# Kernel tuning notes

Measured on AMD Instinct MI355X. Metric: run time of the kernel, lower is better.

## Reference

```python
import jax, jax.numpy as jnp
import numpy as np

N, E, F, H, O, G = 50000, 800000, 50, 512, 121, 20
EPS = 1e-5


def _lin(k, out_f, in_f):
    return jax.random.normal(k, (out_f, in_f), jnp.float32) / np.sqrt(in_f)


def setup_inputs() -> dict:
    key = jax.random.key(0)
    ks = jax.random.split(key, 32)
    inp = {
        "x": jax.random.normal(ks[0], (N, F), jnp.float32),
        "edge_index": jax.random.randint(ks[1], (2, E), 0, N, jnp.int64 if jax.config.jax_enable_x64 else jnp.int32),
        "batch": jnp.sort(jax.random.randint(ks[2], (N,), 0, G, jnp.int32)),
    }
    dims = [(F, H), (H, H), (H, H), (H, H), (H, O)]
    ki = 3
    for i, (fi, fo) in enumerate(dims, start=1):
        inp[f"W{i}l"] = _lin(ks[ki], fo, fi); ki += 1
        inp[f"W{i}r"] = _lin(ks[ki], fo, fi); ki += 1
        inp[f"b{i}"] = jnp.zeros((fo,), jnp.float32)
    for i in range(1, 5):
        inp[f"g{i}"] = jnp.ones((H,), jnp.float32)    # GraphNorm weight
        inp[f"bn{i}"] = jnp.zeros((H,), jnp.float32)  # GraphNorm bias
        inp[f"a{i}"] = jnp.ones((H,), jnp.float32)    # GraphNorm mean_scale
    return inp


def _sage(x, src, dst, inv_deg, Wl, Wr, b):
    # mean aggregation of neighbor messages x[src] at dst, then two linears
    agg = jax.ops.segment_sum(x[src], dst, num_segments=N) * inv_deg  # [N, Fin]
    return agg @ Wl.T + x @ Wr.T + b


def _gnorm(x, batch, inv_sz, w, b, alpha):
    mean = jax.ops.segment_sum(x, batch, num_segments=G) * inv_sz  # [G, C]
    out = x - alpha * mean[batch]
    var = jax.ops.segment_sum(out * out, batch, num_segments=G) * inv_sz
    return out * jax.lax.rsqrt(var[batch] + EPS) * w + b


def reference(x, edge_index, batch,
              W1l, W1r, b1, W2l, W2r, b2, W3l, W3r, b3, W4l, W4r, b4, W5l, W5r, b5,
              g1, bn1, a1, g2, bn2, a2, g3, bn3, a3, g4, bn4, a4):
    src, dst = edge_index[0], edge_index[1]
    deg = jax.ops.segment_sum(jnp.ones((E,), jnp.float32), dst, num_segments=N)
    inv_deg = (1.0 / jnp.maximum(deg, 1.0))[:, None]
    sz = jax.ops.segment_sum(jnp.ones((N,), jnp.float32), batch, num_segments=G)
    inv_sz = (1.0 / jnp.maximum(sz, 1.0))[:, None]

    h = _sage(x, src, dst, inv_deg, W1l, W1r, b1)
    h = jax.nn.relu(_gnorm(h, batch, inv_sz, g1, bn1, a1))  # dropout=identity (eval)
    h = _sage(h, src, dst, inv_deg, W2l, W2r, b2)
    h = jax.nn.relu(_gnorm(h, batch, inv_sz, g2, bn2, a2))
    h = _sage(h, src, dst, inv_deg, W3l, W3r, b3)
    h = jax.nn.relu(_gnorm(h, batch, inv_sz, g3, bn3, a3))
    h = _sage(h, src, dst, inv_deg, W4l, W4r, b4)
    h = jax.nn.relu(_gnorm(h, batch, inv_sz, g4, bn4, a4))
    return _sage(h, src, dst, inv_deg, W5l, W5r, b5)
```

## Files before the change

kernel.cpp:

```cpp
#include <hip/hip_runtime.h>
#include <cstddef>
#include <cstdint>

#define N_NODES 50000
#define N_EDGES 800000
#define F_IN 50
#define K1PAD 64
#define H_DIM 512
#define O_DIM 121
#define N_GROUPS 20
#define EPSV 1e-5f
#define M_PAD 50048
#define M_TILES 391

#define SCAN_BLK 256
#define SCAN_NBLK ((N_NODES + SCAN_BLK - 1) / SCAN_BLK)
#define WALL_EL 1769472
#define XB_EL (M_PAD * K1PAD)

typedef unsigned short u16;
typedef __attribute__((ext_vector_type(8))) short short8;
typedef __attribute__((ext_vector_type(8))) unsigned short u16x8;
typedef __attribute__((ext_vector_type(4))) float f32x4;

__device__ __forceinline__ float b2f(u16 u) {
  union { unsigned int i; float f; } v; v.i = ((unsigned int)u) << 16; return v.f;
}
__device__ __forceinline__ u16 f2b(float f) {
  union { float f; unsigned int i; } v; v.f = f;
  unsigned int x = v.i;
  return (u16)((x + 0x7fffu + ((x >> 16) & 1u)) >> 16);
}

__device__ __forceinline__ void gl_lds16(const void* g, void* l) {
  __builtin_amdgcn_global_load_lds(
      (__attribute__((address_space(1))) void*)(g),
      (__attribute__((address_space(3))) void*)(l), 16, 0, 0);
}


__global__ void k_deg(const int* __restrict__ dst, int* __restrict__ deg) {
  int e = blockIdx.x * blockDim.x + threadIdx.x;
  if (e < N_EDGES) atomicAdd(&deg[dst[e]], 1);
}

__global__ void k_scan1(const int* __restrict__ deg, int* __restrict__ off,
                        int* __restrict__ bsum) {
  __shared__ int buf[SCAN_BLK];
  int gid = blockIdx.x * SCAN_BLK + threadIdx.x;
  buf[threadIdx.x] = (gid < N_NODES) ? deg[gid] : 0;
  __syncthreads();
  for (int d = 1; d < SCAN_BLK; d <<= 1) {
    int t = (threadIdx.x >= d) ? buf[threadIdx.x - d] : 0;
    __syncthreads();
    buf[threadIdx.x] += t;
    __syncthreads();
  }
  if (gid < N_NODES) off[gid + 1] = buf[threadIdx.x];
  if (threadIdx.x == SCAN_BLK - 1) bsum[blockIdx.x] = buf[threadIdx.x];
}

__global__ void k_scan2_gbounds(int* __restrict__ bsum, const int* __restrict__ batch,
                                int* __restrict__ gstart, float* __restrict__ inv_sz) {
  int t = threadIdx.x;
  if (blockIdx.x == 0) {
    __shared__ int buf[256];
    buf[t] = (t < SCAN_NBLK) ? bsum[t] : 0;
    __syncthreads();
    for (int d = 1; d < 256; d <<= 1) {
      int v = (t >= d) ? buf[t - d] : 0;
      __syncthreads();
      buf[t] += v;
      __syncthreads();
    }
    if (t < SCAN_NBLK) bsum[t] = buf[t];
  } else {
    if (t <= N_GROUPS) {
      int lo = 0, hi = N_NODES;
      while (lo < hi) {
        int mid = (lo + hi) >> 1;
        if (batch[mid] < t) lo = mid + 1; else hi = mid;
      }
      gstart[t] = lo;
    }
    __syncthreads();
    if (t < N_GROUPS) {
      int sz = gstart[t + 1] - gstart[t];
      inv_sz[t] = 1.0f / (float)max(sz, 1);
    }
  }
}

__global__ void k_scan3prep(int* __restrict__ off, const int* __restrict__ bsum,
                            const int* __restrict__ deg, float* __restrict__ inv_deg,
                            int* __restrict__ cursor) {
  int gid = blockIdx.x * SCAN_BLK + threadIdx.x;
  if (gid < N_NODES) {
    int add = (blockIdx.x > 0) ? bsum[blockIdx.x - 1] : 0;
    int v = off[gid + 1] + add;
    off[gid + 1] = v;
    if (gid + 1 < N_NODES) cursor[gid + 1] = v;
    inv_deg[gid] = 1.0f / (float)max(deg[gid], 1);
  }
  if (gid == 0) { off[0] = 0; cursor[0] = 0; }
}

__global__ void k_scatter(const int* __restrict__ src, const int* __restrict__ dst,
                          int* __restrict__ cursor, int* __restrict__ csr_src) {
  int e = blockIdx.x * blockDim.x + threadIdx.x;
  if (e < N_EDGES) {
    int p = atomicAdd(&cursor[dst[e]], 1);
    csr_src[p] = src[e];
  }
}

struct WcSrc { const float* p[10]; };
__global__ void k_convert_all(const float* __restrict__ x, WcSrc s,
                              u16* __restrict__ xb, u16* __restrict__ wall) {
  int idx = blockIdx.x * blockDim.x + threadIdx.x;
  if (idx < XB_EL) {
    int r = idx >> 6, c = idx & (K1PAD - 1);
    float v = (r < N_NODES && c < F_IN) ? x[r * F_IN + c] : 0.f;
    xb[idx] = f2b(v);
    return;
  }
  idx -= XB_EL;
  if (idx >= WALL_EL) return;
  const int seg_start[10] = {0, 32768, 65536, 327680, 589824, 851968,
                             1114112, 1376256, 1638400, 1703936};
  const int jr[10]  = {512, 512, 512, 512, 512, 512, 512, 512, 121, 121};
  const int kin[10] = {50, 50, 512, 512, 512, 512, 512, 512, 512, 512};
  const int ksh[10] = {6, 6, 9, 9, 9, 9, 9, 9, 9, 9};
  int sgi = 0;
#pragma unroll
  for (int t = 1; t < 10; ++t)
    if (idx >= seg_start[t]) sgi = t;
  int local = idx - seg_start[sgi];
  int j = local >> ksh[sgi];
  int k = local & ((1 << ksh[sgi]) - 1);
  float v = (j < jr[sgi] && k < kin[sgi]) ? s.p[sgi][j * kin[sgi] + k] : 0.f;
  wall[idx] = f2b(v);
}


__global__ void k_agg_small(const u16* __restrict__ xb, const int* __restrict__ off,
                            const int* __restrict__ srcs, const float* __restrict__ inv_deg,
                            u16* __restrict__ agg) {
  int n = blockIdx.x;
  int f = threadIdx.x;
  int b = off[n], e = off[n + 1];
  float s = 0.f;
  for (int i = b; i < e; ++i) s += b2f(xb[(size_t)srcs[i] * K1PAD + f]);
  agg[(size_t)n * K1PAD + f] = f2b(s * inv_deg[n]);
}

__global__ __launch_bounds__(512) void k_agg512(
    const u16* __restrict__ h, const int* __restrict__ off,
    const int* __restrict__ srcs, const float* __restrict__ inv_deg,
    u16* __restrict__ agg) {
  __shared__ float part[4][64][8];
  int slot = threadIdx.y >> 1;
  int sub = threadIdx.y & 1;
  int n = blockIdx.x * 4 + slot;
  int t = threadIdx.x;
  float a[8] = {0.f, 0.f, 0.f, 0.f, 0.f, 0.f, 0.f, 0.f};
  if (n < N_NODES) {
    int b = off[n], e = off[n + 1];
    int half = (e - b + 1) >> 1;
    int lo = b + sub * half;
    int hi = min(lo + half, e);
    int i = lo;
    for (; i + 4 <= hi; i += 4) {
      u16x8 v0 = ((const u16x8*)(h + (size_t)srcs[i + 0] * H_DIM))[t];
      u16x8 v1 = ((const u16x8*)(h + (size_t)srcs[i + 1] * H_DIM))[t];
      u16x8 v2 = ((const u16x8*)(h + (size_t)srcs[i + 2] * H_DIM))[t];
      u16x8 v3 = ((const u16x8*)(h + (size_t)srcs[i + 3] * H_DIM))[t];
#pragma unroll
      for (int j = 0; j < 8; ++j)
        a[j] += (b2f(v0[j]) + b2f(v1[j])) + (b2f(v2[j]) + b2f(v3[j]));
    }
    for (; i < hi; ++i) {
      u16x8 v0 = ((const u16x8*)(h + (size_t)srcs[i] * H_DIM))[t];
#pragma unroll
      for (int j = 0; j < 8; ++j) a[j] += b2f(v0[j]);
    }
  }
  if (sub == 1) {
#pragma unroll
    for (int j = 0; j < 8; ++j) part[slot][t][j] = a[j];
  }
  __syncthreads();
  if (sub == 0 && n < N_NODES) {
    float w = inv_deg[n];
    u16x8 r;
#pragma unroll
    for (int j = 0; j < 8; ++j) r[j] = f2b((a[j] + part[slot][t][j]) * w);
    ((u16x8*)(agg + (size_t)n * H_DIM))[t] = r;
  }
}

__global__ __launch_bounds__(256) void k_agg_final(
    const u16* __restrict__ Plb, const float* __restrict__ Prf,
    const int* __restrict__ off, const int* __restrict__ srcs,
    const float* __restrict__ inv_deg, const float* __restrict__ bias,
    float* __restrict__ out) {
  int n = blockIdx.x * 8 + (threadIdx.x >> 5);
  if (n >= N_NODES) return;
  int l = threadIdx.x & 31;
  int c0 = l * 4;
  int b = off[n], e = off[n + 1];
  float a0 = 0.f, a1 = 0.f, a2 = 0.f, a3 = 0.f;
  int i = b;
  for (; i + 2 <= e; i += 2) {
    ushort4 v0 = ((const ushort4*)(Plb + (size_t)srcs[i] * 128))[l];
    ushort4 v1 = ((const ushort4*)(Plb + (size_t)srcs[i + 1] * 128))[l];
    a0 += b2f(v0.x) + b2f(v1.x); a1 += b2f(v0.y) + b2f(v1.y);
    a2 += b2f(v0.z) + b2f(v1.z); a3 += b2f(v0.w) + b2f(v1.w);
  }
  if (i < e) {
    ushort4 v0 = ((const ushort4*)(Plb + (size_t)srcs[i] * 128))[l];
    a0 += b2f(v0.x); a1 += b2f(v0.y); a2 += b2f(v0.z); a3 += b2f(v0.w);
  }
  float w = inv_deg[n];
  float4 pr = ((const float4*)(Prf + (size_t)n * 128))[l];
  float r0 = a0 * w + pr.x, r1 = a1 * w + pr.y;
  float r2 = a2 * w + pr.z, r3 = a3 * w + pr.w;
  size_t ob = (size_t)n * O_DIM;
  if (c0 + 0 < O_DIM) out[ob + c0 + 0] = r0 + bias[c0 + 0];
  if (c0 + 1 < O_DIM) out[ob + c0 + 1] = r1 + bias[c0 + 1];
  if (c0 + 2 < O_DIM) out[ob + c0 + 2] = r2 + bias[c0 + 2];
  if (c0 + 3 < O_DIM) out[ob + c0 + 3] = r3 + bias[c0 + 3];
}


#define TM 128
#define TK 32

template <int JB, bool DUAL, int OUTMODE>
__global__ __launch_bounds__(256, 4) void k_gemm_mfma(
    const u16* __restrict__ A, const u16* __restrict__ X,
    const u16* __restrict__ Wl, const u16* __restrict__ Wr,
    const float* __restrict__ bias, void* __restrict__ C0,
    void* __restrict__ C1, const int* __restrict__ batch,
    float* __restrict__ ssum, float* __restrict__ ssq, int K) {
  __shared__ u16 As[TM * TK];
  __shared__ u16 Ls[TM * TK];
  __shared__ u16 Xs[DUAL ? TM * TK : 1];
  __shared__ u16 Rs[DUAL ? TM * TK : 1];

  int id = blockIdx.x;
  const int nfull = (M_TILES >> 3) * 8 * JB;
  int m_t, j_t;
  if (id < nfull) {
    m_t = (id / (8 * JB)) * 8 + (id & 7);
    j_t = (id >> 3) & (JB - 1);
  } else {
    int rem = id - nfull;
    const int nrem = M_TILES & 7;
    m_t = (M_TILES & ~7) + rem % nrem;
    j_t = rem / nrem;
  }
  int m0 = m_t * TM;
  int j0 = j_t * 128;

  int tid = threadIdx.x;
  int lane = tid & 63;
  int wave = tid >> 6;
  int quad = lane >> 4;
  int lr = lane & 15;
  int wm = (wave & 1) * 64;
  int wn = (wave >> 1) * 64;

  f32x4 acc[4][4] = {};

  int sr = tid >> 2;
  int sc = (tid & 3) * 8;
  size_t moff0 = (size_t)(m0 + sr) * K + sc;
  size_t moff1 = moff0 + (size_t)64 * K;
  size_t joff0 = (size_t)(j0 + sr) * K + sc;
  size_t joff1 = joff0 + (size_t)64 * K;
  const int dofs = tid * 8;

  for (int k0 = 0; k0 < K; k0 += TK) {
    __syncthreads();
    gl_lds16(A + moff0 + k0, As + dofs);
    gl_lds16(A + moff1 + k0, As + 2048 + dofs);
    gl_lds16(Wl + joff0 + k0, Ls + dofs);
    gl_lds16(Wl + joff1 + k0, Ls + 2048 + dofs);
    if constexpr (DUAL) {
      gl_lds16(X + moff0 + k0, Xs + dofs);
      gl_lds16(X + moff1 + k0, Xs + 2048 + dofs);
      gl_lds16(Wr + joff0 + k0, Rs + dofs);
      gl_lds16(Wr + joff1 + k0, Rs + 2048 + dofs);
    }
    __syncthreads();
    {
      short8 af[4], lf[4];
#pragma unroll
      for (int t = 0; t < 4; ++t) {
        af[t] = *(const short8*)(As + (wm + t * 16 + lr) * TK + quad * 8);
        lf[t] = *(const short8*)(Ls + (wn + t * 16 + lr) * TK + quad * 8);
      }
#pragma unroll
      for (int ti = 0; ti < 4; ++ti)
#pragma unroll
        for (int tj = 0; tj < 4; ++tj)
          acc[ti][tj] = __builtin_amdgcn_mfma_f32_16x16x32_bf16(
              af[ti], lf[tj], acc[ti][tj], 0, 0, 0);
    }
    if constexpr (DUAL) {
      short8 xf[4], rf[4];
#pragma unroll
      for (int t = 0; t < 4; ++t) {
        xf[t] = *(const short8*)(Xs + (wm + t * 16 + lr) * TK + quad * 8);
        rf[t] = *(const short8*)(Rs + (wn + t * 16 + lr) * TK + quad * 8);
      }
#pragma unroll
      for (int ti = 0; ti < 4; ++ti)
#pragma unroll
        for (int tj = 0; tj < 4; ++tj)
          acc[ti][tj] = __builtin_amdgcn_mfma_f32_16x16x32_bf16(
              xf[ti], rf[tj], acc[ti][tj], 0, 0, 0);
    }
  }

  if constexpr (OUTMODE == 0) {
    int glo = batch[m0];
    int lastrow = m0 + TM - 1;
    bool fast = (lastrow < N_NODES) && (batch[lastrow] == glo);
#pragma unroll
    for (int tj = 0; tj < 4; ++tj) {
      int gcol = j0 + wn + tj * 16 + lr;
      float bv = bias[gcol];
      float s = 0.f, q = 0.f;
#pragma unroll
      for (int ti = 0; ti < 4; ++ti) {
        f32x4 v = acc[ti][tj];
        int rbase = m0 + wm + ti * 16 + quad * 4;
        if (fast) {
#pragma unroll
          for (int r = 0; r < 4; ++r) {
            float val = v[r] + bv;
            ((u16*)C0)[(size_t)(rbase + r) * H_DIM + gcol] = f2b(val);
            s += val; q += val * val;
          }
        } else {
          if (rbase + 3 < N_NODES && batch[rbase] == batch[rbase + 3]) {
            float s4 = 0.f, q4 = 0.f;
#pragma unroll
            for (int r = 0; r < 4; ++r) {
              float val = v[r] + bv;
              ((u16*)C0)[(size_t)(rbase + r) * H_DIM + gcol] = f2b(val);
              s4 += val; q4 += val * val;
            }
            int g = batch[rbase];
            atomicAdd(&ssum[g * H_DIM + gcol], s4);
            atomicAdd(&ssq[g * H_DIM + gcol], q4);
          } else {
#pragma unroll
            for (int r = 0; r < 4; ++r) {
              int grow = rbase + r;
              if (grow < N_NODES) {
                float val = v[r] + bv;
                ((u16*)C0)[(size_t)grow * H_DIM + gcol] = f2b(val);
                int g = batch[grow];
                atomicAdd(&ssum[g * H_DIM + gcol], val);
                atomicAdd(&ssq[g * H_DIM + gcol], val * val);
              }
            }
          }
        }
      }
      if (fast) {
        s += __shfl_xor(s, 16); s += __shfl_xor(s, 32);
        q += __shfl_xor(q, 16); q += __shfl_xor(q, 32);
        if (quad == 0) {
          atomicAdd(&ssum[glo * H_DIM + gcol], s);
          atomicAdd(&ssq[glo * H_DIM + gcol], q);
        }
      }
    }
  } else {
#pragma unroll
    for (int tj = 0; tj < 4; ++tj) {
      int gcol = j0 + wn + tj * 16 + lr;
#pragma unroll
      for (int ti = 0; ti < 4; ++ti) {
        f32x4 v = acc[ti][tj];
#pragma unroll
        for (int r = 0; r < 4; ++r) {
          int grow = m0 + wm + ti * 16 + quad * 4 + r;
          if (gcol < 128)
            ((u16*)C0)[(size_t)grow * 128 + gcol] = f2b(v[r]);
          else
            ((float*)C1)[(size_t)grow * 128 + (gcol - 128)] = v[r];
        }
      }
    }
  }
}


__global__ void k_precomp(const float* __restrict__ ssum, const float* __restrict__ ssq,
                          const float* __restrict__ inv_sz, const float* __restrict__ gw,
                          const float* __restrict__ gb, const float* __restrict__ alpha,
                          float* __restrict__ S, float* __restrict__ T) {
  int idx = blockIdx.x * blockDim.x + threadIdx.x;
  if (idx >= N_GROUPS * H_DIM) return;
  int g = idx >> 9;
  int c = idx & (H_DIM - 1);
  float is = inv_sz[g];
  float m = ssum[idx] * is;
  float a = alpha[c];
  float var = fmaxf(ssq[idx] * is - a * (2.f - a) * m * m, 0.f);
  float inv = rsqrtf(var + EPSV);
  float sc = inv * gw[c];
  S[idx] = sc;
  T[idx] = gb[c] - a * m * sc;
}

__global__ void k_apply(u16* __restrict__ h, const int* __restrict__ batch,
                        const float* __restrict__ S, const float* __restrict__ T) {
  int tid = blockIdx.x * blockDim.x + threadIdx.x;
  if (tid >= N_NODES * (H_DIM / 8)) return;
  int n = tid >> 6;
  int c0 = (tid & 63) << 3;
  int g = batch[n];
  u16x8 hv = *(const u16x8*)(h + (size_t)n * H_DIM + c0);
  u16x8 out;
#pragma unroll
  for (int j = 0; j < 8; ++j) {
    int f = c0 + j;
    float y = b2f(hv[j]) * S[g * H_DIM + f] + T[g * H_DIM + f];
    out[j] = f2b(fmaxf(y, 0.f));
  }
  *(u16x8*)(h + (size_t)n * H_DIM + c0) = out;
}


extern "C" void kernel_launch(void* const* d_in, const int* in_sizes, int n_in,
                              void* d_out, int out_size, void* d_ws, size_t ws_size,
                              hipStream_t stream) {
  const float* x = (const float*)d_in[0];
  const int* edge = (const int*)d_in[1];
  const int* batch = (const int*)d_in[2];
  const float *Wl[5], *Wr[5], *bb[5];
  for (int i = 0; i < 5; ++i) {
    Wl[i] = (const float*)d_in[3 + 3 * i];
    Wr[i] = (const float*)d_in[4 + 3 * i];
    bb[i] = (const float*)d_in[5 + 3 * i];
  }
  const float *gamma[4], *beta[4], *alpha[4];
  for (int i = 0; i < 4; ++i) {
    gamma[i] = (const float*)d_in[18 + 3 * i];
    beta[i]  = (const float*)d_in[19 + 3 * i];
    alpha[i] = (const float*)d_in[20 + 3 * i];
  }
  const int* srcv = edge;
  const int* dstv = edge + N_EDGES;

  char* base = (char*)d_ws;
  size_t off = 0;
  auto carve = [&](size_t bytes) -> char* {
    char* p = base + off;
    off = (off + bytes + 255) & ~(size_t)255;
    return p;
  };
  int* deg       = (int*)carve((size_t)N_NODES * 4);
  float* inv_deg = (float*)carve((size_t)N_NODES * 4);
  int* csr_off   = (int*)carve((size_t)(N_NODES + 1) * 4);
  int* cursor    = (int*)carve((size_t)N_NODES * 4);
  int* csr_src   = (int*)carve((size_t)N_EDGES * 4);
  int* bsum      = (int*)carve((size_t)SCAN_NBLK * 4);
  int* gstart    = (int*)carve((size_t)(N_GROUPS + 1) * 4);
  float* inv_sz  = (float*)carve((size_t)N_GROUPS * 4);
  float* stats   = (float*)carve((size_t)4 * 2 * N_GROUPS * H_DIM * 4);
  float* Sbuf    = (float*)carve((size_t)N_GROUPS * H_DIM * 4);
  float* Tbuf    = (float*)carve((size_t)N_GROUPS * H_DIM * 4);
  u16* xb        = (u16*)carve((size_t)XB_EL * 2);
  u16* aggx      = (u16*)carve((size_t)XB_EL * 2);
  u16* h0        = (u16*)carve((size_t)M_PAD * H_DIM * 2);
  u16* h1        = (u16*)carve((size_t)M_PAD * H_DIM * 2);
  u16* h2        = (u16*)carve((size_t)M_PAD * H_DIM * 2);
  u16* wall      = (u16*)carve((size_t)WALL_EL * 2);
  (void)ws_size; (void)in_sizes; (void)n_in; (void)out_size;

  u16* w1lb = wall;
  u16* w1rb = wall + 32768;
  u16* w2lb = wall + 65536;
  u16* w2rb = wall + 327680;
  u16* w3lb = wall + 589824;
  u16* w3rb = wall + 851968;
  u16* w4lb = wall + 1114112;
  u16* w4rb = wall + 1376256;
  u16* w5cat = wall + 1638400;

  u16* Plb = h1;
  float* Prf = (float*)((char*)h1 + (size_t)M_PAD * 128 * 2);

  hipMemsetAsync(deg, 0, (size_t)N_NODES * 4, stream);
  k_deg<<<(N_EDGES + 255) / 256, 256, 0, stream>>>(dstv, deg);
  k_scan1<<<SCAN_NBLK, SCAN_BLK, 0, stream>>>(deg, csr_off, bsum);
  k_scan2_gbounds<<<2, 256, 0, stream>>>(bsum, batch, gstart, inv_sz);
  k_scan3prep<<<SCAN_NBLK, SCAN_BLK, 0, stream>>>(csr_off, bsum, deg, inv_deg, cursor);
  k_scatter<<<(N_EDGES + 255) / 256, 256, 0, stream>>>(srcv, dstv, cursor, csr_src);

  WcSrc ws_src;
  ws_src.p[0] = Wl[0]; ws_src.p[1] = Wr[0];
  ws_src.p[2] = Wl[1]; ws_src.p[3] = Wr[1];
  ws_src.p[4] = Wl[2]; ws_src.p[5] = Wr[2];
  ws_src.p[6] = Wl[3]; ws_src.p[7] = Wr[3];
  ws_src.p[8] = Wl[4]; ws_src.p[9] = Wr[4];
  k_convert_all<<<(XB_EL + WALL_EL + 255) / 256, 256, 0, stream>>>(x, ws_src, xb, wall);

  hipMemsetAsync(stats, 0, (size_t)4 * 2 * N_GROUPS * H_DIM * 4, stream);

  const int nblk_main = M_TILES * 4;
  const int nblk_l5   = M_TILES * 2;
  dim3 aggblk(64, 8);
  int aggrid = (N_NODES + 3) / 4;

  auto norm = [&](u16* h, int l) {
    float* ss = stats + (size_t)l * 2 * N_GROUPS * H_DIM;
    float* sq = ss + N_GROUPS * H_DIM;
    k_precomp<<<(N_GROUPS * H_DIM + 255) / 256, 256, 0, stream>>>(
        ss, sq, inv_sz, gamma[l], beta[l], alpha[l], Sbuf, Tbuf);
    k_apply<<<(N_NODES * (H_DIM / 8) + 255) / 256, 256, 0, stream>>>(
        h, batch, Sbuf, Tbuf);
  };
  auto stat_ptr = [&](int l) { return stats + (size_t)l * 2 * N_GROUPS * H_DIM; };

  k_agg_small<<<N_NODES, 64, 0, stream>>>(xb, csr_off, csr_src, inv_deg, aggx);
  k_gemm_mfma<4, true, 0><<<nblk_main, 256, 0, stream>>>(
      aggx, xb, w1lb, w1rb, bb[0], h0, nullptr, batch,
      stat_ptr(0), stat_ptr(0) + N_GROUPS * H_DIM, K1PAD);
  norm(h0, 0);

  k_agg512<<<aggrid, aggblk, 0, stream>>>(h0, csr_off, csr_src, inv_deg, h1);
  k_gemm_mfma<4, true, 0><<<nblk_main, 256, 0, stream>>>(
      h1, h0, w2lb, w2rb, bb[1], h2, nullptr, batch,
      stat_ptr(1), stat_ptr(1) + N_GROUPS * H_DIM, H_DIM);
  norm(h2, 1);

  k_agg512<<<aggrid, aggblk, 0, stream>>>(h2, csr_off, csr_src, inv_deg, h0);
  k_gemm_mfma<4, true, 0><<<nblk_main, 256, 0, stream>>>(
      h0, h2, w3lb, w3rb, bb[2], h1, nullptr, batch,
      stat_ptr(2), stat_ptr(2) + N_GROUPS * H_DIM, H_DIM);
  norm(h1, 2);

  k_agg512<<<aggrid, aggblk, 0, stream>>>(h1, csr_off, csr_src, inv_deg, h2);
  k_gemm_mfma<4, true, 0><<<nblk_main, 256, 0, stream>>>(
      h2, h1, w4lb, w4rb, bb[3], h0, nullptr, batch,
      stat_ptr(3), stat_ptr(3) + N_GROUPS * H_DIM, H_DIM);
  norm(h0, 3);

  k_gemm_mfma<2, false, 1><<<nblk_l5, 256, 0, stream>>>(
      h0, nullptr, w5cat, nullptr, nullptr, Plb, Prf, nullptr, nullptr, nullptr, H_DIM);
  k_agg_final<<<(N_NODES + 7) / 8, 256, 0, stream>>>(
      Plb, Prf, csr_off, csr_src, inv_deg, bb[4], (float*)d_out);
}
```

Measured before the change: 1.071 ms.

## Add 256x256-tile 8-wave MFMA GEMM with interleaved double-buffered staging

Adds a new GEMM kernel using 256x256 output tiles and 512 threads, with double-buffered LDS and staged global-to-LDS loads interleaved between four MFMA sub-phases. It replaces the older GEMM for layers 2-4 and the final projection, and pads M to a multiple of 256. Larger tiles raise arithmetic intensity and cut operand reloads. The cost is higher register and LDS pressure and fewer blocks (392 for the main layers), which may under-fill the device and cause tail imbalance.

```diff
diff --git a/kernel.cpp b/kernel.cpp
--- a/kernel.cpp
+++ b/kernel.cpp
@@ -10,8 +10,9 @@
 #define O_DIM 121
 #define N_GROUPS 20
 #define EPSV 1e-5f
-#define M_PAD 50048
-#define M_TILES 391
+#define M_PAD 50176
+#define M_TILES 392
+#define M_TILES256 196
 
 #define SCAN_BLK 256
 #define SCAN_NBLK ((N_NODES + SCAN_BLK - 1) / SCAN_BLK)
@@ -396,6 +397,240 @@
             ((float*)C1)[(size_t)grow * 128 + (gcol - 128)] = v[r];
         }
       }
+    }
+  }
+}
+
+
+template <int OUTMODE>
+__global__ __launch_bounds__(512, 2) void k_gemm256(
+    const u16* __restrict__ Aa, const u16* __restrict__ Ax,
+    const u16* __restrict__ Bl, const u16* __restrict__ Br,
+    const float* __restrict__ bias, void* __restrict__ C0,
+    void* __restrict__ C1, const int* __restrict__ batch,
+    float* __restrict__ ssum, float* __restrict__ ssq, int knt) {
+  __shared__ u16 LA[2][256][64];
+  __shared__ u16 LB[2][256][64];
+
+  int m_t, j_t;
+  if constexpr (OUTMODE == 0) {
+    int lg = (blockIdx.x & 7) * 49 + (blockIdx.x >> 3);
+    m_t = lg >> 1; j_t = lg & 1;
+  } else {
+    m_t = blockIdx.x; j_t = 0;
+  }
+  const int m0 = m_t << 8;
+  const int j0 = j_t << 8;
+
+  const int tid = threadIdx.x;
+  const int lane = tid & 63;
+  const int wave = tid >> 6;
+  const int lr = lane & 15;
+  const int quad = lane >> 4;
+  const int wr64 = ((wave >> 2) & 1) << 6;
+  const int wc64 = (wave & 3) << 6;
+  const int rtid = tid >> 3;
+  const int sw = ((tid & 7) ^ (rtid & 7)) << 3;
+  const int c16_0 = (quad << 3) ^ ((lr & 7) << 3);
+  const int c16_1 = (32 + (quad << 3)) ^ ((lr & 7) << 3);
+
+  f32x4 acc[2][4][4] = {};
+  short8 af[4][2];
+  short8 bf[4][2];
+
+  auto STAGE = [&](int tt, int kind) {
+    if (tt >= knt) return;
+    const int bb = tt & 1;
+    const int ktl = (tt & 7) << 6;
+    if (kind <= 1) {
+      const u16* src = (tt >= 8) ? Ax : Aa;
+      const int r0 = kind << 7;
+      const u16* s0 = src + (size_t)(m0 + r0 + rtid) * 512 + ktl + sw;
+      u16* d = &LA[bb][r0][0] + tid * 8;
+      gl_lds16(s0, d);
+      gl_lds16(s0 + (size_t)64 * 512, d + 4096);
+    } else {
+      const u16* src = (tt >= 8) ? Br : Bl;
+      const int r0 = (kind - 2) << 7;
+      const u16* s0 = src + (size_t)(j0 + r0 + rtid) * 512 + ktl + sw;
+      u16* d = &LB[bb][r0][0] + tid * 8;
+      gl_lds16(s0, d);
+      gl_lds16(s0 + (size_t)64 * 512, d + 4096);
+    }
+  };
+
+  STAGE(0, 0); STAGE(0, 2); STAGE(0, 3); STAGE(0, 1);
+  STAGE(1, 0); STAGE(1, 2); STAGE(1, 3);
+  asm volatile("s_waitcnt vmcnt(6)" ::: "memory");
+  __builtin_amdgcn_s_barrier();
+
+  for (int t = 0; t < knt; ++t) {
+    const int b = t & 1;
+    const u16* ABase = &LA[b][0][0];
+    const u16* BBase = &LB[b][0][0];
+    const u16* abr = ABase + (size_t)(wr64 + lr) * 64;
+    const u16* bbr = BBase + (size_t)(wc64 + lr) * 64;
+
+#pragma unroll
+    for (int mi = 0; mi < 4; ++mi) {
+      af[mi][0] = *(const short8*)(abr + mi * 1024 + c16_0);
+      af[mi][1] = *(const short8*)(abr + mi * 1024 + c16_1);
+    }
+#pragma unroll
+    for (int nj = 0; nj < 2; ++nj) {
+      bf[nj][0] = *(const short8*)(bbr + nj * 1024 + c16_0);
+      bf[nj][1] = *(const short8*)(bbr + nj * 1024 + c16_1);
+    }
+    STAGE(t + 1, 1);
+    __builtin_amdgcn_s_barrier();
+    __builtin_amdgcn_s_setprio(1);
+#pragma unroll
+    for (int mi = 0; mi < 4; ++mi)
+#pragma unroll
+      for (int nj = 0; nj < 2; ++nj) {
+        acc[0][mi][nj] = __builtin_amdgcn_mfma_f32_16x16x32_bf16(
+            af[mi][0], bf[nj][0], acc[0][mi][nj], 0, 0, 0);
+        acc[0][mi][nj] = __builtin_amdgcn_mfma_f32_16x16x32_bf16(
+            af[mi][1], bf[nj][1], acc[0][mi][nj], 0, 0, 0);
+      }
+    __builtin_amdgcn_s_setprio(0);
+    __builtin_amdgcn_s_barrier();
+
+#pragma unroll
+    for (int nj = 2; nj < 4; ++nj) {
+      bf[nj][0] = *(const short8*)(bbr + nj * 1024 + c16_0);
+      bf[nj][1] = *(const short8*)(bbr + nj * 1024 + c16_1);
+    }
+    STAGE(t + 2, 0);
+    __builtin_amdgcn_s_barrier();
+    __builtin_amdgcn_s_setprio(1);
+#pragma unroll
+    for (int mi = 0; mi < 4; ++mi)
+#pragma unroll
+      for (int nj = 2; nj < 4; ++nj) {
+        acc[0][mi][nj] = __builtin_amdgcn_mfma_f32_16x16x32_bf16(
+            af[mi][0], bf[nj][0], acc[0][mi][nj], 0, 0, 0);
+        acc[0][mi][nj] = __builtin_amdgcn_mfma_f32_16x16x32_bf16(
+            af[mi][1], bf[nj][1], acc[0][mi][nj], 0, 0, 0);
+      }
+    __builtin_amdgcn_s_setprio(0);
+    __builtin_amdgcn_s_barrier();
+
+#pragma unroll
+    for (int mi = 0; mi < 4; ++mi) {
+      af[mi][0] = *(const short8*)(abr + 8192 + mi * 1024 + c16_0);
+      af[mi][1] = *(const short8*)(abr + 8192 + mi * 1024 + c16_1);
+    }
+    STAGE(t + 2, 2);
+    __builtin_amdgcn_s_barrier();
+    __builtin_amdgcn_s_setprio(1);
+#pragma unroll
+    for (int mi = 0; mi < 4; ++mi)
+#pragma unroll
+      for (int nj = 0; nj < 2; ++nj) {
+        acc[1][mi][nj] = __builtin_amdgcn_mfma_f32_16x16x32_bf16(
+            af[mi][0], bf[nj][0], acc[1][mi][nj], 0, 0, 0);
+        acc[1][mi][nj] = __builtin_amdgcn_mfma_f32_16x16x32_bf16(
+            af[mi][1], bf[nj][1], acc[1][mi][nj], 0, 0, 0);
+      }
+    __builtin_amdgcn_s_setprio(0);
+    __builtin_amdgcn_s_barrier();
+
+    STAGE(t + 2, 3);
+    if (t < knt - 2) {
+      asm volatile("s_waitcnt vmcnt(6)" ::: "memory");
+    } else if (t == knt - 2) {
+      asm volatile("s_waitcnt vmcnt(0)" ::: "memory");
+    }
+    __builtin_amdgcn_s_barrier();
+    __builtin_amdgcn_s_setprio(1);
+#pragma unroll
+    for (int mi = 0; mi < 4; ++mi)
+#pragma unroll
+      for (int nj = 2; nj < 4; ++nj) {
+        acc[1][mi][nj] = __builtin_amdgcn_mfma_f32_16x16x32_bf16(
+            af[mi][0], bf[nj][0], acc[1][mi][nj], 0, 0, 0);
+        acc[1][mi][nj] = __builtin_amdgcn_mfma_f32_16x16x32_bf16(
+            af[mi][1], bf[nj][1], acc[1][mi][nj], 0, 0, 0);
+      }
+    __builtin_amdgcn_s_setprio(0);
+    __builtin_amdgcn_s_barrier();
+  }
+
+  if constexpr (OUTMODE == 0) {
+    int glo = batch[m0];
+    int lastrow = m0 + 255;
+    bool fast = (lastrow < N_NODES) && (batch[lastrow] == glo);
+#pragma unroll
+    for (int nj = 0; nj < 4; ++nj) {
+      int gcol = j0 + wc64 + nj * 16 + lr;
+      float bv = bias[gcol];
+      float s = 0.f, q = 0.f;
+#pragma unroll
+      for (int band = 0; band < 2; ++band)
+#pragma unroll
+        for (int mi = 0; mi < 4; ++mi) {
+          f32x4 v = acc[band][mi][nj];
+          int rbase = m0 + band * 128 + wr64 + mi * 16 + quad * 4;
+          if (fast) {
+#pragma unroll
+            for (int r = 0; r < 4; ++r) {
+              float val = v[r] + bv;
+              ((u16*)C0)[(size_t)(rbase + r) * H_DIM + gcol] = f2b(val);
+              s += val; q += val * val;
+            }
+          } else if (rbase + 3 < N_NODES && batch[rbase] == batch[rbase + 3]) {
+            float s4 = 0.f, q4 = 0.f;
+#pragma unroll
+            for (int r = 0; r < 4; ++r) {
+              float val = v[r] + bv;
+              ((u16*)C0)[(size_t)(rbase + r) * H_DIM + gcol] = f2b(val);
+              s4 += val; q4 += val * val;
+            }
+            int g = batch[rbase];
+            atomicAdd(&ssum[g * H_DIM + gcol], s4);
+            atomicAdd(&ssq[g * H_DIM + gcol], q4);
+          } else {
+#pragma unroll
+            for (int r = 0; r < 4; ++r) {
+              int grow = rbase + r;
+              if (grow < N_NODES) {
+                float val = v[r] + bv;
+                ((u16*)C0)[(size_t)grow * H_DIM + gcol] = f2b(val);
+                int g = batch[grow];
+                atomicAdd(&ssum[g * H_DIM + gcol], val);
+                atomicAdd(&ssq[g * H_DIM + gcol], val * val);
+              }
+            }
+          }
+        }
+      if (fast) {
+        s += __shfl_xor(s, 16); s += __shfl_xor(s, 32);
+        q += __shfl_xor(q, 16); q += __shfl_xor(q, 32);
+        if (quad == 0) {
+          atomicAdd(&ssum[glo * H_DIM + gcol], s);
+          atomicAdd(&ssq[glo * H_DIM + gcol], q);
+        }
+      }
+    }
+  } else {
+#pragma unroll
+    for (int nj = 0; nj < 4; ++nj) {
+      int gcol = wc64 + nj * 16 + lr;
+#pragma unroll
+      for (int band = 0; band < 2; ++band)
+#pragma unroll
+        for (int mi = 0; mi < 4; ++mi) {
+          f32x4 v = acc[band][mi][nj];
+#pragma unroll
+          for (int r = 0; r < 4; ++r) {
+            int grow = m0 + band * 128 + wr64 + mi * 16 + quad * 4 + r;
+            if (gcol < 128)
+              ((u16*)C0)[(size_t)grow * 128 + gcol] = f2b(v[r]);
+            else
+              ((float*)C1)[(size_t)grow * 128 + (gcol - 128)] = v[r];
+          }
+        }
     }
   }
 }
@@ -515,8 +750,8 @@
 
   hipMemsetAsync(stats, 0, (size_t)4 * 2 * N_GROUPS * H_DIM * 4, stream);
 
-  const int nblk_main = M_TILES * 4;
-  const int nblk_l5   = M_TILES * 2;
+  const int nblk_l1 = M_TILES * 4;
+  const int nblk_256 = M_TILES256 * 2;
   dim3 aggblk(64, 8);
   int aggrid = (N_NODES + 3) / 4;
 
@@ -531,31 +766,31 @@
   auto stat_ptr = [&](int l) { return stats + (size_t)l * 2 * N_GROUPS * H_DIM; };
 
   k_agg_small<<<N_NODES, 64, 0, stream>>>(xb, csr_off, csr_src, inv_deg, aggx);
-  k_gemm_mfma<4, true, 0><<<nblk_main, 256, 0, stream>>>(
+  k_gemm_mfma<4, true, 0><<<nblk_l1, 256, 0, stream>>>(
       aggx, xb, w1lb, w1rb, bb[0], h0, nullptr, batch,
       stat_ptr(0), stat_ptr(0) + N_GROUPS * H_DIM, K1PAD);
   norm(h0, 0);
 
   k_agg512<<<aggrid, aggblk, 0, stream>>>(h0, csr_off, csr_src, inv_deg, h1);
-  k_gemm_mfma<4, true, 0><<<nblk_main, 256, 0, stream>>>(
+  k_gemm256<0><<<nblk_256, 512, 0, stream>>>(
       h1, h0, w2lb, w2rb, bb[1], h2, nullptr, batch,
-      stat_ptr(1), stat_ptr(1) + N_GROUPS * H_DIM, H_DIM);
+      stat_ptr(1), stat_ptr(1) + N_GROUPS * H_DIM, 16);
   norm(h2, 1);
 
   k_agg512<<<aggrid, aggblk, 0, stream>>>(h2, csr_off, csr_src, inv_deg, h0);
-  k_gemm_mfma<4, true, 0><<<nblk_main, 256, 0, stream>>>(
+  k_gemm256<0><<<nblk_256, 512, 0, stream>>>(
       h0, h2, w3lb, w3rb, bb[2], h1, nullptr, batch,
-      stat_ptr(2), stat_ptr(2) + N_GROUPS * H_DIM, H_DIM);
+      stat_ptr(2), stat_ptr(2) + N_GROUPS * H_DIM, 16);
   norm(h1, 2);
 
   k_agg512<<<aggrid, aggblk, 0, stream>>>(h1, csr_off, csr_src, inv_deg, h2);
-  k_gemm_mfma<4, true, 0><<<nblk_main, 256, 0, stream>>>(
+  k_gemm256<0><<<nblk_256, 512, 0, stream>>>(
       h2, h1, w4lb, w4rb, bb[3], h0, nullptr, batch,
-      stat_ptr(3), stat_ptr(3) + N_GROUPS * H_DIM, H_DIM);
+      stat_ptr(3), stat_ptr(3) + N_GROUPS * H_DIM, 16);
   norm(h0, 3);
 
-  k_gemm_mfma<2, false, 1><<<nblk_l5, 256, 0, stream>>>(
-      h0, nullptr, w5cat, nullptr, nullptr, Plb, Prf, nullptr, nullptr, nullptr, H_DIM);
+  k_gemm256<1><<<M_TILES256, 512, 0, stream>>>(
+      h0, h0, w5cat, w5cat, nullptr, Plb, Prf, nullptr, nullptr, nullptr, 8);
   k_agg_final<<<(N_NODES + 7) / 8, 256, 0, stream>>>(
       Plb, Prf, csr_off, csr_src, inv_deg, bb[4], (float*)d_out);
 }
```

Result: slower. 1.134 ms (+5.9%).

## Store activations in column-sliced layout and aggregate per slice per XCD

Applied to the files above, without the earlier changes.

Normalized activations are now written in a layout split into 16 column slices of 32 features, each slice contiguous over nodes. A new aggregation kernel assigns two slices to each XCD (by block index modulo 8), so each XCD's gather working set is a small slice that can stay cache-resident instead of whole 1 KB rows. The GEMM gains a sliced-layout mode for reading A and X, and M_PAD is padded to a multiple of 8 tiles. The cost is 64-byte (ushort4) gathers with shuffle reductions, and correctness relies on the hardware distributing blocks to XCDs round-robin.

```diff
diff --git a/kernel.cpp b/kernel.cpp
--- a/kernel.cpp
+++ b/kernel.cpp
@@ -10,8 +10,8 @@
 #define O_DIM 121
 #define N_GROUPS 20
 #define EPSV 1e-5f
-#define M_PAD 50048
-#define M_TILES 391
+#define M_PAD 50176
+#define M_TILES 392
 
 #define SCAN_BLK 256
 #define SCAN_NBLK ((N_NODES + SCAN_BLK - 1) / SCAN_BLK)
@@ -154,48 +154,46 @@
   agg[(size_t)n * K1PAD + f] = f2b(s * inv_deg[n]);
 }
 
-__global__ __launch_bounds__(512) void k_agg512(
-    const u16* __restrict__ h, const int* __restrict__ off,
+#define AGG_BLKS 1024
+__global__ __launch_bounds__(256) void k_agg_slice(
+    const u16* __restrict__ hs, const int* __restrict__ off,
     const int* __restrict__ srcs, const float* __restrict__ inv_deg,
-    u16* __restrict__ agg) {
-  __shared__ float part[4][64][8];
-  int slot = threadIdx.y >> 1;
-  int sub = threadIdx.y & 1;
-  int n = blockIdx.x * 4 + slot;
-  int t = threadIdx.x;
-  float a[8] = {0.f, 0.f, 0.f, 0.f, 0.f, 0.f, 0.f, 0.f};
-  if (n < N_NODES) {
-    int b = off[n], e = off[n + 1];
-    int half = (e - b + 1) >> 1;
-    int lo = b + sub * half;
-    int hi = min(lo + half, e);
-    int i = lo;
-    for (; i + 4 <= hi; i += 4) {
-      u16x8 v0 = ((const u16x8*)(h + (size_t)srcs[i + 0] * H_DIM))[t];
-      u16x8 v1 = ((const u16x8*)(h + (size_t)srcs[i + 1] * H_DIM))[t];
-      u16x8 v2 = ((const u16x8*)(h + (size_t)srcs[i + 2] * H_DIM))[t];
-      u16x8 v3 = ((const u16x8*)(h + (size_t)srcs[i + 3] * H_DIM))[t];
-#pragma unroll
-      for (int j = 0; j < 8; ++j)
-        a[j] += (b2f(v0[j]) + b2f(v1[j])) + (b2f(v2[j]) + b2f(v3[j]));
-    }
-    for (; i < hi; ++i) {
-      u16x8 v0 = ((const u16x8*)(h + (size_t)srcs[i] * H_DIM))[t];
-#pragma unroll
-      for (int j = 0; j < 8; ++j) a[j] += b2f(v0[j]);
-    }
-  }
-  if (sub == 1) {
-#pragma unroll
-    for (int j = 0; j < 8; ++j) part[slot][t][j] = a[j];
-  }
-  __syncthreads();
-  if (sub == 0 && n < N_NODES) {
-    float w = inv_deg[n];
-    u16x8 r;
-#pragma unroll
-    for (int j = 0; j < 8; ++j) r[j] = f2b((a[j] + part[slot][t][j]) * w);
-    ((u16x8*)(agg + (size_t)n * H_DIM))[t] = r;
+    u16* __restrict__ aggs) {
+  const int xcd = blockIdx.x & 7;
+  const int chunk = blockIdx.x >> 3;
+  const int nchunk = AGG_BLKS / 8;
+  const int per = (N_NODES + nchunk - 1) / nchunk;
+  const int n0 = chunk * per;
+  const int n1 = min(n0 + per, N_NODES);
+  const int wave = threadIdx.x >> 6;
+  const int lane = threadIdx.x & 63;
+  const int eidx = lane >> 3;
+  const int sub = lane & 7;
+#pragma unroll
+  for (int ph = 0; ph < 2; ++ph) {
+    const int s = xcd * 2 + ph;
+    const u16* hsl = hs + (size_t)s * M_PAD * 32 + sub * 4;
+    u16* asl = aggs + (size_t)s * M_PAD * 32 + sub * 4;
+    for (int n = n0 + wave; n < n1; n += 4) {
+      int b = off[n], e = off[n + 1];
+      float a0 = 0.f, a1 = 0.f, a2 = 0.f, a3 = 0.f;
+      for (int i = b + eidx; i < e; i += 8) {
+        ushort4 v = *(const ushort4*)(hsl + (size_t)srcs[i] * 32);
+        a0 += b2f(v.x); a1 += b2f(v.y); a2 += b2f(v.z); a3 += b2f(v.w);
+      }
+#pragma unroll
+      for (int m = 8; m <= 32; m <<= 1) {
+        a0 += __shfl_xor(a0, m); a1 += __shfl_xor(a1, m);
+        a2 += __shfl_xor(a2, m); a3 += __shfl_xor(a3, m);
+      }
+      if (eidx == 0) {
+        float w = inv_deg[n];
+        ushort4 r;
+        r.x = f2b(a0 * w); r.y = f2b(a1 * w);
+        r.z = f2b(a2 * w); r.w = f2b(a3 * w);
+        *(ushort4*)(asl + (size_t)n * 32) = r;
+      }
+    }
   }
 }
 
@@ -236,7 +234,7 @@
 #define TM 128
 #define TK 32
 
-template <int JB, bool DUAL, int OUTMODE>
+template <int JB, bool DUAL, int OUTMODE, bool SL>
 __global__ __launch_bounds__(256, 4) void k_gemm_mfma(
     const u16* __restrict__ A, const u16* __restrict__ X,
     const u16* __restrict__ Wl, const u16* __restrict__ Wr,
@@ -256,7 +254,7 @@
     j_t = (id >> 3) & (JB - 1);
   } else {
     int rem = id - nfull;
-    const int nrem = M_TILES & 7;
+    const int nrem = (M_TILES & 7) ? (M_TILES & 7) : 1;
     m_t = (M_TILES & ~7) + rem % nrem;
     j_t = rem / nrem;
   }
@@ -275,24 +273,32 @@
 
   int sr = tid >> 2;
   int sc = (tid & 3) * 8;
-  size_t moff0 = (size_t)(m0 + sr) * K + sc;
-  size_t moff1 = moff0 + (size_t)64 * K;
+  const size_t kstep = SL ? (size_t)M_PAD * 32 : (size_t)TK;
+  const size_t rstep = SL ? (size_t)64 * 32 : (size_t)64 * K;
+  const u16* Ap = A + (SL ? (size_t)(m0 + sr) * 32 + sc
+                          : (size_t)(m0 + sr) * K + sc);
+  const u16* Xp = nullptr;
+  if constexpr (DUAL)
+    Xp = X + (SL ? (size_t)(m0 + sr) * 32 + sc
+                 : (size_t)(m0 + sr) * K + sc);
   size_t joff0 = (size_t)(j0 + sr) * K + sc;
   size_t joff1 = joff0 + (size_t)64 * K;
   const int dofs = tid * 8;
 
   for (int k0 = 0; k0 < K; k0 += TK) {
     __syncthreads();
-    gl_lds16(A + moff0 + k0, As + dofs);
-    gl_lds16(A + moff1 + k0, As + 2048 + dofs);
+    gl_lds16(Ap, As + dofs);
+    gl_lds16(Ap + rstep, As + 2048 + dofs);
     gl_lds16(Wl + joff0 + k0, Ls + dofs);
     gl_lds16(Wl + joff1 + k0, Ls + 2048 + dofs);
     if constexpr (DUAL) {
-      gl_lds16(X + moff0 + k0, Xs + dofs);
-      gl_lds16(X + moff1 + k0, Xs + 2048 + dofs);
+      gl_lds16(Xp, Xs + dofs);
+      gl_lds16(Xp + rstep, Xs + 2048 + dofs);
       gl_lds16(Wr + joff0 + k0, Rs + dofs);
       gl_lds16(Wr + joff1 + k0, Rs + 2048 + dofs);
-    }
+      Xp += kstep;
+    }
+    Ap += kstep;
     __syncthreads();
     {
       short8 af[4], lf[4];
@@ -419,14 +425,15 @@
   T[idx] = gb[c] - a * m * sc;
 }
 
-__global__ void k_apply(u16* __restrict__ h, const int* __restrict__ batch,
+__global__ void k_apply(const u16* __restrict__ praw, u16* __restrict__ hs,
+                        const int* __restrict__ batch,
                         const float* __restrict__ S, const float* __restrict__ T) {
   int tid = blockIdx.x * blockDim.x + threadIdx.x;
   if (tid >= N_NODES * (H_DIM / 8)) return;
   int n = tid >> 6;
   int c0 = (tid & 63) << 3;
   int g = batch[n];
-  u16x8 hv = *(const u16x8*)(h + (size_t)n * H_DIM + c0);
+  u16x8 hv = *(const u16x8*)(praw + (size_t)n * H_DIM + c0);
   u16x8 out;
 #pragma unroll
   for (int j = 0; j < 8; ++j) {
@@ -434,7 +441,7 @@
     float y = b2f(hv[j]) * S[g * H_DIM + f] + T[g * H_DIM + f];
     out[j] = f2b(fmaxf(y, 0.f));
   }
-  *(u16x8*)(h + (size_t)n * H_DIM + c0) = out;
+  *(u16x8*)(hs + ((size_t)(c0 >> 5) * M_PAD + n) * 32 + (c0 & 31)) = out;
 }
 
 
@@ -479,9 +486,9 @@
   float* Tbuf    = (float*)carve((size_t)N_GROUPS * H_DIM * 4);
   u16* xb        = (u16*)carve((size_t)XB_EL * 2);
   u16* aggx      = (u16*)carve((size_t)XB_EL * 2);
-  u16* h0        = (u16*)carve((size_t)M_PAD * H_DIM * 2);
-  u16* h1        = (u16*)carve((size_t)M_PAD * H_DIM * 2);
-  u16* h2        = (u16*)carve((size_t)M_PAD * H_DIM * 2);
+  u16* praw      = (u16*)carve((size_t)M_PAD * H_DIM * 2);
+  u16* hsA       = (u16*)carve((size_t)M_PAD * H_DIM * 2);
+  u16* aggs      = (u16*)carve((size_t)M_PAD * H_DIM * 2);
   u16* wall      = (u16*)carve((size_t)WALL_EL * 2);
   (void)ws_size; (void)in_sizes; (void)n_in; (void)out_size;
 
@@ -495,8 +502,8 @@
   u16* w4rb = wall + 1376256;
   u16* w5cat = wall + 1638400;
 
-  u16* Plb = h1;
-  float* Prf = (float*)((char*)h1 + (size_t)M_PAD * 128 * 2);
+  u16* Plb = aggs;
+  float* Prf = (float*)((char*)aggs + (size_t)M_PAD * 128 * 2);
 
   hipMemsetAsync(deg, 0, (size_t)N_NODES * 4, stream);
   k_deg<<<(N_EDGES + 255) / 256, 256, 0, stream>>>(dstv, deg);
@@ -517,45 +524,43 @@
 
   const int nblk_main = M_TILES * 4;
   const int nblk_l5   = M_TILES * 2;
-  dim3 aggblk(64, 8);
-  int aggrid = (N_NODES + 3) / 4;
-
-  auto norm = [&](u16* h, int l) {
+
+  auto norm = [&](int l) {
     float* ss = stats + (size_t)l * 2 * N_GROUPS * H_DIM;
     float* sq = ss + N_GROUPS * H_DIM;
     k_precomp<<<(N_GROUPS * H_DIM + 255) / 256, 256, 0, stream>>>(
         ss, sq, inv_sz, gamma[l], beta[l], alpha[l], Sbuf, Tbuf);
     k_apply<<<(N_NODES * (H_DIM / 8) + 255) / 256, 256, 0, stream>>>(
-        h, batch, Sbuf, Tbuf);
+        praw, hsA, batch, Sbuf, Tbuf);
   };
   auto stat_ptr = [&](int l) { return stats + (size_t)l * 2 * N_GROUPS * H_DIM; };
 
   k_agg_small<<<N_NODES, 64, 0, stream>>>(xb, csr_off, csr_src, inv_deg, aggx);
-  k_gemm_mfma<4, true, 0><<<nblk_main, 256, 0, stream>>>(
-      aggx, xb, w1lb, w1rb, bb[0], h0, nullptr, batch,
+  k_gemm_mfma<4, true, 0, false><<<nblk_main, 256, 0, stream>>>(
+      aggx, xb, w1lb, w1rb, bb[0], praw, nullptr, batch,
       stat_ptr(0), stat_ptr(0) + N_GROUPS * H_DIM, K1PAD);
-  norm(h0, 0);
-
-  k_agg512<<<aggrid, aggblk, 0, stream>>>(h0, csr_off, csr_src, inv_deg, h1);
-  k_gemm_mfma<4, true, 0><<<nblk_main, 256, 0, stream>>>(
-      h1, h0, w2lb, w2rb, bb[1], h2, nullptr, batch,
+  norm(0);
+
+  k_agg_slice<<<AGG_BLKS, 256, 0, stream>>>(hsA, csr_off, csr_src, inv_deg, aggs);
+  k_gemm_mfma<4, true, 0, true><<<nblk_main, 256, 0, stream>>>(
+      aggs, hsA, w2lb, w2rb, bb[1], praw, nullptr, batch,
       stat_ptr(1), stat_ptr(1) + N_GROUPS * H_DIM, H_DIM);
-  norm(h2, 1);
-
-  k_agg512<<<aggrid, aggblk, 0, stream>>>(h2, csr_off, csr_src, inv_deg, h0);
-  k_gemm_mfma<4, true, 0><<<nblk_main, 256, 0, stream>>>(
-      h0, h2, w3lb, w3rb, bb[2], h1, nullptr, batch,
+  norm(1);
+
+  k_agg_slice<<<AGG_BLKS, 256, 0, stream>>>(hsA, csr_off, csr_src, inv_deg, aggs);
+  k_gemm_mfma<4, true, 0, true><<<nblk_main, 256, 0, stream>>>(
+      aggs, hsA, w3lb, w3rb, bb[2], praw, nullptr, batch,
       stat_ptr(2), stat_ptr(2) + N_GROUPS * H_DIM, H_DIM);
-  norm(h1, 2);
-
-  k_agg512<<<aggrid, aggblk, 0, stream>>>(h1, csr_off, csr_src, inv_deg, h2);
-  k_gemm_mfma<4, true, 0><<<nblk_main, 256, 0, stream>>>(
-      h2, h1, w4lb, w4rb, bb[3], h0, nullptr, batch,
+  norm(2);
+
+  k_agg_slice<<<AGG_BLKS, 256, 0, stream>>>(hsA, csr_off, csr_src, inv_deg, aggs);
+  k_gemm_mfma<4, true, 0, true><<<nblk_main, 256, 0, stream>>>(
+      aggs, hsA, w4lb, w4rb, bb[3], praw, nullptr, batch,
       stat_ptr(3), stat_ptr(3) + N_GROUPS * H_DIM, H_DIM);
-  norm(h0, 3);
-
-  k_gemm_mfma<2, false, 1><<<nblk_l5, 256, 0, stream>>>(
-      h0, nullptr, w5cat, nullptr, nullptr, Plb, Prf, nullptr, nullptr, nullptr, H_DIM);
+  norm(3);
+
+  k_gemm_mfma<2, false, 1, true><<<nblk_l5, 256, 0, stream>>>(
+      hsA, nullptr, w5cat, nullptr, nullptr, Plb, Prf, nullptr, nullptr, nullptr, H_DIM);
   k_agg_final<<<(N_NODES + 7) / 8, 256, 0, stream>>>(
       Plb, Prf, csr_off, csr_src, inv_deg, bb[4], (float*)d_out);
 }
```

New measurement: 1.775 ms. +65.8%, slower.
